# Optimization experiments

Measured on AMD Instinct MI355X. Metric: run time of the kernel, lower is better.

## Reference

```python
import jax, jax.numpy as jnp
import numpy as np

NUM_LAYERS = 12
D = 256          # d_model
H = 8            # n_head
DK = D // H      # qk_dim = v_dim = 32
FFD = 1024       # ffd_dim
B, L = 32, 448
EPS = 1e-6
MAXLEN = 500


def _sinusoidal_pos_emb(maxlen, hidden_dim):
    depth = hidden_dim / 2
    positions = np.arange(maxlen, dtype=np.float32)[:, None]
    depths = np.arange(depth, dtype=np.float32)[None, :] / depth
    angle_rads = positions * (1.0 / np.power(10000.0, depths))
    pe = np.concatenate([np.sin(angle_rads), np.cos(angle_rads)], axis=-1)
    return jnp.asarray(pe, jnp.float32)


def setup_inputs() -> dict:
    key = jax.random.key(0)
    ks = jax.random.split(key, 16)
    s = 0.02
    inp = {
        "x": jax.random.normal(ks[0], (B, L, D), jnp.float32),
        "mask": jnp.zeros((B, L), jnp.bool_),
        "pos_emb": _sinusoidal_pos_emb(MAXLEN - 1, D)[:L],  # [L, D]
        "Wq": jax.random.normal(ks[1], (NUM_LAYERS, D, D), jnp.float32) * s,
        "bq": jnp.zeros((NUM_LAYERS, D), jnp.float32),
        "Wk": jax.random.normal(ks[2], (NUM_LAYERS, D, D), jnp.float32) * s,
        "bk": jnp.zeros((NUM_LAYERS, D), jnp.float32),
        "Wv": jax.random.normal(ks[3], (NUM_LAYERS, D, D), jnp.float32) * s,
        "bv": jnp.zeros((NUM_LAYERS, D), jnp.float32),
        "Wo": jax.random.normal(ks[4], (NUM_LAYERS, D, D), jnp.float32) * s,
        "bo": jnp.zeros((NUM_LAYERS, D), jnp.float32),
        "W1": jax.random.normal(ks[5], (NUM_LAYERS, D, FFD), jnp.float32) * s,
        "bf1": jnp.zeros((NUM_LAYERS, FFD), jnp.float32),
        "W2": jax.random.normal(ks[6], (NUM_LAYERS, FFD, D), jnp.float32) * s,
        "bf2": jnp.zeros((NUM_LAYERS, D), jnp.float32),
        "ln1_g": jnp.ones((NUM_LAYERS, D), jnp.float32),
        "ln1_b": jnp.zeros((NUM_LAYERS, D), jnp.float32),
        "ln2_g": jnp.ones((NUM_LAYERS, D), jnp.float32),
        "ln2_b": jnp.zeros((NUM_LAYERS, D), jnp.float32),
    }
    return inp


def _layer_norm(x, g, b):
    mu = jnp.mean(x, axis=-1, keepdims=True)
    var = jnp.mean(jnp.square(x - mu), axis=-1, keepdims=True)
    return (x - mu) * jax.lax.rsqrt(var + EPS) * g + b


def _encoder_forward(x, mask, pos_emb, Wq, bq, Wk, bk, Wv, bv, Wo, bo,
                     W1, bf1, W2, bf2, ln1_g, ln1_b, ln2_g, ln2_b):
    Bx, Lx, _ = x.shape
    scale = 1.0 / np.sqrt(DK)
    x = x + pos_emb[None, :Lx, :]
    mask_b = mask[:, None, None, :]  # [B,1,1,L], True = masked
    for i in range(NUM_LAYERS):
        # --- pre-norm attention ---
        nx = _layer_norm(x, ln1_g[i], ln1_b[i])
        q = (nx @ Wq[i] + bq[i]).reshape(Bx, Lx, H, DK)
        k = (nx @ Wk[i] + bk[i]).reshape(Bx, Lx, H, DK)
        v = (nx @ Wv[i] + bv[i]).reshape(Bx, Lx, H, DK)
        dot = jnp.einsum("bihd,bjhd->bhij", q, k) * scale
        dot = jnp.where(mask_b, -10000.0, dot)
        attn = jax.nn.softmax(dot, axis=-1)
        o = jnp.einsum("bhij,bjhd->bihd", attn, v).reshape(Bx, Lx, D)
        x = x + (o @ Wo[i] + bo[i])
        # --- pre-norm FFN (exact GELU, as torch nn.GELU) ---
        nx2 = _layer_norm(x, ln2_g[i], ln2_b[i])
        h = jax.nn.gelu(nx2 @ W1[i] + bf1[i], approximate=False)
        x = x + (h @ W2[i] + bf2[i])
    return x


def reference(x, mask, pos_emb, Wq, bq, Wk, bk, Wv, bv, Wo, bo,
              W1, bf1, W2, bf2, ln1_g, ln1_b, ln2_g, ln2_b):
    return _encoder_forward(x, mask, pos_emb, Wq, bq, Wk, bk, Wv, bv, Wo, bo,
                            W1, bf1, W2, bf2, ln1_g, ln1_b, ln2_g, ln2_b)
```

## Files before the change

kernel.cpp:

```cpp
#include <hip/hip_runtime.h>

#define NL 12
#define DM 256
#define FFDIM 1024
#define BBATCH 32
#define LSEQ 448
#define MTOK (BBATCH*LSEQ)
#define EPSF 1e-6f

typedef __attribute__((ext_vector_type(8))) short bf16x8;
typedef __attribute__((ext_vector_type(4))) float f32x4;
typedef unsigned short u16;
typedef unsigned int u32;

__device__ __forceinline__ u16 f2bf(float f) {
    union { float f; u32 u; } v; v.f = f;
    u32 r = v.u + 0x7fffu + ((v.u >> 16) & 1u);
    return (u16)(r >> 16);
}
__device__ __forceinline__ float gelu_exact(float x) {
    return 0.5f * x * (1.0f + erff(x * 0.70710678118654752f));
}
__device__ __forceinline__ void gload16(const u16* g, u16* l) {
    __builtin_amdgcn_global_load_lds(
        (const __attribute__((address_space(1))) u32*)g,
        (__attribute__((address_space(3))) u32*)l, 16, 0, 0);
}

__global__ __launch_bounds__(256) void add_pos_k(
    const float* __restrict__ x, const float* __restrict__ pe, float* __restrict__ out)
{
    int i = blockIdx.x * 256 + threadIdx.x;
    float4 xv = ((const float4*)x)[i];
    float4 pv = ((const float4*)pe)[i % (LSEQ * DM / 4)];
    float4 r;
    r.x = xv.x + pv.x; r.y = xv.y + pv.y; r.z = xv.z + pv.z; r.w = xv.w + pv.w;
    ((float4*)out)[i] = r;
}

__global__ __launch_bounds__(256) void ln_k(
    const float* __restrict__ x, const float* __restrict__ g,
    const float* __restrict__ b, u16* __restrict__ out)
{
    const int w = threadIdx.x >> 6, lane = threadIdx.x & 63;
    const int row = blockIdx.x * 4 + w;
    float4 v = ((const float4*)(x + (size_t)row * DM))[lane];
    float s = v.x + v.y + v.z + v.w;
#pragma unroll
    for (int off = 32; off; off >>= 1) s += __shfl_xor(s, off);
    float mu = s * (1.0f / 256.0f);
    float d0 = v.x - mu, d1 = v.y - mu, d2 = v.z - mu, d3 = v.w - mu;
    float sq = d0*d0 + d1*d1 + d2*d2 + d3*d3;
#pragma unroll
    for (int off = 32; off; off >>= 1) sq += __shfl_xor(sq, off);
    float rs = rsqrtf(sq * (1.0f / 256.0f) + EPSF);
    float4 gv = ((const float4*)g)[lane];
    float4 bv = ((const float4*)b)[lane];
    ushort4 o;
    o.x = f2bf(d0 * rs * gv.x + bv.x);
    o.y = f2bf(d1 * rs * gv.y + bv.y);
    o.z = f2bf(d2 * rs * gv.z + bv.z);
    o.w = f2bf(d3 * rs * gv.w + bv.w);
    *(ushort4*)(out + (size_t)row * DM + lane * 4) = o;
}

__global__ __launch_bounds__(256) void twt_k(
    const float* __restrict__ in, u16* __restrict__ out,
    int K, int N, int in_lstride, int out_lstride)
{
    __shared__ float tl[32][33];
    const int l = blockIdx.z;
    const int n0 = blockIdx.x * 32, k0 = blockIdx.y * 32;
    const int tx = threadIdx.x & 31, ty = threadIdx.x >> 5;
    const float* src = in + (size_t)l * in_lstride;
#pragma unroll
    for (int i = 0; i < 4; ++i)
        tl[ty + 8*i][tx] = src[(size_t)(k0 + ty + 8*i) * N + n0 + tx];
    __syncthreads();
    u16* dst = out + (size_t)l * out_lstride;
#pragma unroll
    for (int i = 0; i < 4; ++i)
        dst[(size_t)(n0 + ty + 8*i) * K + k0 + tx] = f2bf(tl[tx][ty + 8*i]);
}

__global__ __launch_bounds__(256) void pack_bias_k(
    const float* __restrict__ bq, const float* __restrict__ bk,
    const float* __restrict__ bv, float* __restrict__ bqkv)
{
    int i = blockIdx.x * 256 + threadIdx.x;
    if (i >= NL * 768) return;
    int l = i / 768, c = i % 768;
    float v = (c < 256) ? bq[l*256 + c] : (c < 512) ? bk[l*256 + c - 256] : bv[l*256 + c - 512];
    bqkv[i] = v;
}

__global__ __launch_bounds__(256) void vt_k(
    const u16* __restrict__ qkv, u16* __restrict__ vtg)
{
    __shared__ u16 tl[32][33];
    const int kt = blockIdx.x, h = blockIdx.y, b = blockIdx.z;
    const int tx = threadIdx.x & 31, ty = threadIdx.x >> 5;
#pragma unroll
    for (int i = 0; i < 4; ++i)
        tl[ty + 8*i][tx] = qkv[(size_t)(b*LSEQ + kt*32 + ty + 8*i) * 768 + 512 + h*32 + tx];
    __syncthreads();
#pragma unroll
    for (int i = 0; i < 4; ++i)
        vtg[((size_t)(b*8 + h)*32 + ty + 8*i) * 448 + kt*32 + tx] = tl[tx][ty + 8*i];
}

template<int BN, int EPI>
__global__ __launch_bounds__(256, 2) void mm_k(
    const u16* __restrict__ A, int lda, const u16* __restrict__ Bt,
    const float* __restrict__ bias, void* __restrict__ C, int ldc, int K)
{
    __shared__ u16 As[2 * 128 * 32];
    __shared__ u16 Bs[2 * BN * 32];
    constexpr int MT = (BN == 128) ? 4 : 2;
    constexpr int BPANEL = BN * 32;
    const int tid = threadIdx.x;
    const int by = blockIdx.x, bx = blockIdx.y;
    const int w = tid >> 6, lane = tid & 63;
    const int lm = lane & 15, lk = lane >> 4;
    const int wm = (BN == 128) ? (w >> 1) : w;
    const int wn = (BN == 128) ? (w & 1) : 0;
    const int m0 = wm * MT * 16;
    const int n0 = wn * 64;
    const int lrow = lane >> 2, lcol = (lane & 3) * 8;

    const u16* Ab = A + (size_t)(by * 128) * lda;
    const u16* Bb = Bt + (size_t)(bx * BN) * K;

    f32x4 zz = {0.f, 0.f, 0.f, 0.f};
    f32x4 acc[MT][4];
#pragma unroll
    for (int i = 0; i < MT; ++i)
#pragma unroll
        for (int j = 0; j < 4; ++j) acc[i][j] = zz;

    for (int k0 = 0; k0 < K; k0 += 64) {
        __syncthreads();
#pragma unroll
        for (int p = 0; p < 2; ++p) {
#pragma unroll
            for (int i = 0; i < 2; ++i) {
                int seg = w * 2 + i;
                gload16(Ab + (size_t)(seg * 16 + lrow) * lda + k0 + p * 32 + lcol,
                        &As[p * 4096 + seg * 512]);
            }
            if constexpr (BN == 128) {
#pragma unroll
                for (int i = 0; i < 2; ++i) {
                    int seg = w * 2 + i;
                    gload16(Bb + (size_t)(seg * 16 + lrow) * K + k0 + p * 32 + lcol,
                            &Bs[p * BPANEL + seg * 512]);
                }
            } else {
                gload16(Bb + (size_t)(w * 16 + lrow) * K + k0 + p * 32 + lcol,
                        &Bs[p * BPANEL + w * 512]);
            }
        }
        __syncthreads();

#pragma unroll
        for (int p = 0; p < 2; ++p) {
            bf16x8 af[MT], bfr[4];
#pragma unroll
            for (int mt = 0; mt < MT; ++mt)
                af[mt] = *(const bf16x8*)&As[p * 4096 + (m0 + mt*16 + lm)*32 + lk*8];
#pragma unroll
            for (int nt = 0; nt < 4; ++nt)
                bfr[nt] = *(const bf16x8*)&Bs[p * BPANEL + (n0 + nt*16 + lm)*32 + lk*8];
#pragma unroll
            for (int mt = 0; mt < MT; ++mt)
#pragma unroll
                for (int nt = 0; nt < 4; ++nt)
                    acc[mt][nt] = __builtin_amdgcn_mfma_f32_16x16x32_bf16(af[mt], bfr[nt], acc[mt][nt], 0, 0, 0);
        }
    }

    float bv[4];
#pragma unroll
    for (int nt = 0; nt < 4; ++nt) bv[nt] = bias[bx*BN + n0 + nt*16 + lm];
#pragma unroll
    for (int mt = 0; mt < MT; ++mt) {
#pragma unroll
        for (int r = 0; r < 4; ++r) {
            int grow = by*128 + m0 + mt*16 + lk*4 + r;
#pragma unroll
            for (int nt = 0; nt < 4; ++nt) {
                int gcol = bx*BN + n0 + nt*16 + lm;
                float vv = acc[mt][nt][r] + bv[nt];
                if constexpr (EPI == 0) {
                    ((u16*)C)[(size_t)grow * ldc + gcol] = f2bf(vv);
                } else if constexpr (EPI == 1) {
                    ((u16*)C)[(size_t)grow * ldc + gcol] = f2bf(gelu_exact(vv));
                } else {
                    float* p = (float*)C + (size_t)grow * ldc + gcol;
                    *p += vv;
                }
            }
        }
    }
}

__global__ __launch_bounds__(256, 2) void attn_k(
    const u16* __restrict__ qkv, const u16* __restrict__ vtg,
    const unsigned char* __restrict__ mask, u16* __restrict__ ob)
{
    __shared__ u16 Klds[448 * 32];
    __shared__ u16 Plds[4][16 * 68];
    const int tid = threadIdx.x, w = tid >> 6, lane = tid & 63;
    const int lm = lane & 15, lk = lane >> 4;
    const int bid = blockIdx.x;
    const int bh = bid & 255, sg = bid >> 8;
    const int b = bh >> 3, h = bh & 7;
    const size_t rowbase = (size_t)b * LSEQ;

#pragma unroll
    for (int i = 0; i < 7; ++i) {
        int seg = w * 7 + i;
        gload16(qkv + (rowbase + seg * 16 + (lane >> 2)) * 768 + 256 + h * 32 + (lane & 3) * 8,
                &Klds[seg * 512]);
    }
    unsigned mbits = 0;
#pragma unroll
    for (int t = 0; t < 28; ++t)
        mbits |= (mask[b * LSEQ + t * 16 + lm] ? 1u : 0u) << t;
    __syncthreads();

    const u16* Vb = vtg + (size_t)bh * 32 * 448;
    const float scale = 0.17677669529663687f;
    f32x4 zz = {0.f, 0.f, 0.f, 0.f};

    const int q0 = (sg * 4 + w) * 16;
    bf16x8 qf = *(const bf16x8*)(qkv + (rowbase + q0 + lm) * 768 + h * 32 + lk * 8);
    f32x4 sc[28];
#pragma unroll
    for (int t = 0; t < 28; ++t) {
        bf16x8 kf = *(const bf16x8*)&Klds[(t*16 + lm)*32 + lk*8];
        sc[t] = __builtin_amdgcn_mfma_f32_16x16x32_bf16(qf, kf, zz, 0, 0, 0);
    }
    float mx[4] = {-1e30f, -1e30f, -1e30f, -1e30f};
#pragma unroll
    for (int t = 0; t < 28; ++t) {
        bool m = (mbits >> t) & 1;
#pragma unroll
        for (int r = 0; r < 4; ++r) {
            float v = m ? -10000.0f : sc[t][r] * scale;
            sc[t][r] = v;
            mx[r] = fmaxf(mx[r], v);
        }
    }
#pragma unroll
    for (int off = 1; off < 16; off <<= 1)
#pragma unroll
        for (int r = 0; r < 4; ++r) mx[r] = fmaxf(mx[r], __shfl_xor(mx[r], off));
    float sum[4] = {0.f, 0.f, 0.f, 0.f};
#pragma unroll
    for (int t = 0; t < 28; ++t)
#pragma unroll
        for (int r = 0; r < 4; ++r) {
            float e = __expf(sc[t][r] - mx[r]);
            sc[t][r] = e;
            sum[r] += e;
        }
#pragma unroll
    for (int off = 1; off < 16; off <<= 1)
#pragma unroll
        for (int r = 0; r < 4; ++r) sum[r] += __shfl_xor(sum[r], off);
    float inv[4];
#pragma unroll
    for (int r = 0; r < 4; ++r) inv[r] = 1.0f / sum[r];

    f32x4 oacc[2] = {zz, zz};
    u16* P = &Plds[w][0];
#pragma unroll
    for (int cc = 0; cc < 7; ++cc) {
#pragma unroll
        for (int tt = 0; tt < 4; ++tt) {
            int t = cc*4 + tt;
#pragma unroll
            for (int r = 0; r < 4; ++r)
                P[(lk*4 + r)*68 + tt*16 + lm] = f2bf(sc[t][r]);
        }
        bf16x8 pa0 = *(const bf16x8*)&P[lm*68 + lk*8];
        bf16x8 pa1 = *(const bf16x8*)&P[lm*68 + 32 + lk*8];
#pragma unroll
        for (int dt = 0; dt < 2; ++dt) {
            bf16x8 vb0 = *(const bf16x8*)(Vb + (size_t)(dt*16 + lm)*448 + cc*64 + lk*8);
            bf16x8 vb1 = *(const bf16x8*)(Vb + (size_t)(dt*16 + lm)*448 + cc*64 + 32 + lk*8);
            oacc[dt] = __builtin_amdgcn_mfma_f32_16x16x32_bf16(pa0, vb0, oacc[dt], 0, 0, 0);
            oacc[dt] = __builtin_amdgcn_mfma_f32_16x16x32_bf16(pa1, vb1, oacc[dt], 0, 0, 0);
        }
    }
#pragma unroll
    for (int dt = 0; dt < 2; ++dt)
#pragma unroll
        for (int r = 0; r < 4; ++r)
            ob[(rowbase + q0 + lk*4 + r)*256 + h*32 + dt*16 + lm] = f2bf(oacc[dt][r] * inv[r]);
}

extern "C" void kernel_launch(void* const* d_in, const int* in_sizes, int n_in,
                              void* d_out, int out_size, void* d_ws, size_t ws_size,
                              hipStream_t stream)
{
    const float* x_in = (const float*)d_in[0];
    const unsigned char* mask = (const unsigned char*)d_in[1];
    const float* pe   = (const float*)d_in[2];
    const float* Wq = (const float*)d_in[3];
    const float* bq = (const float*)d_in[4];
    const float* Wk = (const float*)d_in[5];
    const float* bk = (const float*)d_in[6];
    const float* Wv = (const float*)d_in[7];
    const float* bv = (const float*)d_in[8];
    const float* Wo = (const float*)d_in[9];
    const float* bo = (const float*)d_in[10];
    const float* W1 = (const float*)d_in[11];
    const float* bf1 = (const float*)d_in[12];
    const float* W2 = (const float*)d_in[13];
    const float* bf2 = (const float*)d_in[14];
    const float* ln1_g = (const float*)d_in[15];
    const float* ln1_b = (const float*)d_in[16];
    const float* ln2_g = (const float*)d_in[17];
    const float* ln2_b = (const float*)d_in[18];

    float* x = (float*)d_out;
    u16* ws = (u16*)d_ws;
    u16* nx   = ws;
    u16* qkv  = nx + 3670016;
    u16* ob   = qkv + 11010048;
    u16* vtg  = ob + 3670016;
    u16* hb   = qkv;
    u16* wqkvt = vtg + 3670016;
    u16* wot  = wqkvt + 2359296;
    u16* w1t  = wot + 786432;
    u16* w2t  = w1t + 3145728;
    float* bqkv = (float*)(w2t + 3145728);

    add_pos_k<<<MTOK * DM / 1024, 256, 0, stream>>>(x_in, pe, x);

    twt_k<<<dim3(8, 8, NL), 256, 0, stream>>>(Wq, wqkvt,          256, 256, 65536, 196608);
    twt_k<<<dim3(8, 8, NL), 256, 0, stream>>>(Wk, wqkvt + 65536,  256, 256, 65536, 196608);
    twt_k<<<dim3(8, 8, NL), 256, 0, stream>>>(Wv, wqkvt + 131072, 256, 256, 65536, 196608);
    twt_k<<<dim3(8, 8, NL), 256, 0, stream>>>(Wo, wot, 256, 256, 65536, 65536);
    twt_k<<<dim3(32, 8, NL), 256, 0, stream>>>(W1, w1t, 256, 1024, 262144, 262144);
    twt_k<<<dim3(8, 32, NL), 256, 0, stream>>>(W2, w2t, 1024, 256, 262144, 262144);
    pack_bias_k<<<(NL * 768 + 255) / 256, 256, 0, stream>>>(bq, bk, bv, bqkv);

    for (int l = 0; l < NL; ++l) {
        ln_k<<<MTOK / 4, 256, 0, stream>>>(x, ln1_g + l*256, ln1_b + l*256, nx);
        mm_k<128, 0><<<dim3(112, 6), 256, 0, stream>>>(
            nx, 256, wqkvt + (size_t)l*196608, bqkv + l*768, qkv, 768, 256);
        vt_k<<<dim3(14, 8, 32), 256, 0, stream>>>(qkv, vtg);
        attn_k<<<1792, 256, 0, stream>>>(qkv, vtg, mask, ob);
        mm_k<64, 2><<<dim3(112, 4), 256, 0, stream>>>(
            ob, 256, wot + (size_t)l*65536, bo + l*256, x, 256, 256);
        ln_k<<<MTOK / 4, 256, 0, stream>>>(x, ln2_g + l*256, ln2_b + l*256, nx);
        mm_k<128, 1><<<dim3(112, 8), 256, 0, stream>>>(
            nx, 256, w1t + (size_t)l*262144, bf1 + l*1024, hb, 1024, 256);
        mm_k<64, 2><<<dim3(112, 4), 256, 0, stream>>>(
            hb, 1024, w2t + (size_t)l*262144, bf2 + l*256, x, 256, 1024);
    }
}
```

Measured before the change: 1.563 ms.

## Recompute attention scores to shrink registers, fold Q scale into QKV GEMM, retile residual GEMMs

The attention kernel stops holding all 28 score tiles in registers. It computes QK^T once to get the row max, then recomputes the scores while exponentiating and feeding P·V. This removes a separate exp pass, and launch bounds are raised to 4 blocks per CU for higher occupancy, at the cost of doubling the QK MFMAs. The 1/sqrt(dk) scale is moved into a new QKV GEMM epilogue that scales the Q columns. The Wo and W2 residual GEMMs switch to 64x64 tiles with twice as many blocks and higher occupancy bounds.

Measured after the change: 1.456 ms. -6.8%, faster.

```diff
diff --git a/kernel.cpp b/kernel.cpp
--- a/kernel.cpp
+++ b/kernel.cpp
@@ -7,6 +7,7 @@
 #define LSEQ 448
 #define MTOK (BBATCH*LSEQ)
 #define EPSF 1e-6f
+#define QSCALE 0.17677669529663687f
 
 typedef __attribute__((ext_vector_type(8))) short bf16x8;
 typedef __attribute__((ext_vector_type(4))) float f32x4;
@@ -109,26 +110,25 @@
         vtg[((size_t)(b*8 + h)*32 + ty + 8*i) * 448 + kt*32 + tx] = tl[tx][ty + 8*i];
 }
 
-template<int BN, int EPI>
-__global__ __launch_bounds__(256, 2) void mm_k(
+template<int BM, int BN, int EPI>
+__global__ __launch_bounds__(256, (BM == 64) ? 4 : 3) void mm_k(
     const u16* __restrict__ A, int lda, const u16* __restrict__ Bt,
     const float* __restrict__ bias, void* __restrict__ C, int ldc, int K)
 {
-    __shared__ u16 As[2 * 128 * 32];
+    __shared__ u16 As[2 * BM * 32];
     __shared__ u16 Bs[2 * BN * 32];
-    constexpr int MT = (BN == 128) ? 4 : 2;
+    constexpr int MT = (BM == 128) ? 4 : 1;
+    constexpr int APANEL = BM * 32;
     constexpr int BPANEL = BN * 32;
     const int tid = threadIdx.x;
     const int by = blockIdx.x, bx = blockIdx.y;
     const int w = tid >> 6, lane = tid & 63;
     const int lm = lane & 15, lk = lane >> 4;
-    const int wm = (BN == 128) ? (w >> 1) : w;
-    const int wn = (BN == 128) ? (w & 1) : 0;
-    const int m0 = wm * MT * 16;
-    const int n0 = wn * 64;
+    const int m0 = (BM == 128) ? ((w >> 1) * 64) : (w * 16);
+    const int n0 = (BM == 128) ? ((w & 1) * 64) : 0;
     const int lrow = lane >> 2, lcol = (lane & 3) * 8;
 
-    const u16* Ab = A + (size_t)(by * 128) * lda;
+    const u16* Ab = A + (size_t)(by * BM) * lda;
     const u16* Bb = Bt + (size_t)(bx * BN) * K;
 
     f32x4 zz = {0.f, 0.f, 0.f, 0.f};
@@ -142,20 +142,18 @@
         __syncthreads();
 #pragma unroll
         for (int p = 0; p < 2; ++p) {
-#pragma unroll
-            for (int i = 0; i < 2; ++i) {
-                int seg = w * 2 + i;
-                gload16(Ab + (size_t)(seg * 16 + lrow) * lda + k0 + p * 32 + lcol,
-                        &As[p * 4096 + seg * 512]);
-            }
-            if constexpr (BN == 128) {
+            if constexpr (BM == 128) {
 #pragma unroll
                 for (int i = 0; i < 2; ++i) {
                     int seg = w * 2 + i;
+                    gload16(Ab + (size_t)(seg * 16 + lrow) * lda + k0 + p * 32 + lcol,
+                            &As[p * APANEL + seg * 512]);
                     gload16(Bb + (size_t)(seg * 16 + lrow) * K + k0 + p * 32 + lcol,
                             &Bs[p * BPANEL + seg * 512]);
                 }
             } else {
+                gload16(Ab + (size_t)(w * 16 + lrow) * lda + k0 + p * 32 + lcol,
+                        &As[p * APANEL + w * 512]);
                 gload16(Bb + (size_t)(w * 16 + lrow) * K + k0 + p * 32 + lcol,
                         &Bs[p * BPANEL + w * 512]);
             }
@@ -167,7 +165,7 @@
             bf16x8 af[MT], bfr[4];
 #pragma unroll
             for (int mt = 0; mt < MT; ++mt)
-                af[mt] = *(const bf16x8*)&As[p * 4096 + (m0 + mt*16 + lm)*32 + lk*8];
+                af[mt] = *(const bf16x8*)&As[p * APANEL + (m0 + mt*16 + lm)*32 + lk*8];
 #pragma unroll
             for (int nt = 0; nt < 4; ++nt)
                 bfr[nt] = *(const bf16x8*)&Bs[p * BPANEL + (n0 + nt*16 + lm)*32 + lk*8];
@@ -186,7 +184,7 @@
     for (int mt = 0; mt < MT; ++mt) {
 #pragma unroll
         for (int r = 0; r < 4; ++r) {
-            int grow = by*128 + m0 + mt*16 + lk*4 + r;
+            int grow = by*BM + m0 + mt*16 + lk*4 + r;
 #pragma unroll
             for (int nt = 0; nt < 4; ++nt) {
                 int gcol = bx*BN + n0 + nt*16 + lm;
@@ -195,6 +193,9 @@
                     ((u16*)C)[(size_t)grow * ldc + gcol] = f2bf(vv);
                 } else if constexpr (EPI == 1) {
                     ((u16*)C)[(size_t)grow * ldc + gcol] = f2bf(gelu_exact(vv));
+                } else if constexpr (EPI == 3) {
+                    float qs = (gcol < 256) ? QSCALE : 1.0f;
+                    ((u16*)C)[(size_t)grow * ldc + gcol] = f2bf(vv * qs);
                 } else {
                     float* p = (float*)C + (size_t)grow * ldc + gcol;
                     *p += vv;
@@ -204,7 +205,7 @@
     }
 }
 
-__global__ __launch_bounds__(256, 2) void attn_k(
+__global__ __launch_bounds__(256, 4) void attn_k(
     const u16* __restrict__ qkv, const u16* __restrict__ vtg,
     const unsigned char* __restrict__ mask, u16* __restrict__ ob)
 {
@@ -230,25 +231,20 @@
     __syncthreads();
 
     const u16* Vb = vtg + (size_t)bh * 32 * 448;
-    const float scale = 0.17677669529663687f;
     f32x4 zz = {0.f, 0.f, 0.f, 0.f};
 
     const int q0 = (sg * 4 + w) * 16;
     bf16x8 qf = *(const bf16x8*)(qkv + (rowbase + q0 + lm) * 768 + h * 32 + lk * 8);
-    f32x4 sc[28];
+
+    float mx[4] = {-1e30f, -1e30f, -1e30f, -1e30f};
 #pragma unroll
     for (int t = 0; t < 28; ++t) {
         bf16x8 kf = *(const bf16x8*)&Klds[(t*16 + lm)*32 + lk*8];
-        sc[t] = __builtin_amdgcn_mfma_f32_16x16x32_bf16(qf, kf, zz, 0, 0, 0);
-    }
-    float mx[4] = {-1e30f, -1e30f, -1e30f, -1e30f};
-#pragma unroll
-    for (int t = 0; t < 28; ++t) {
+        f32x4 s = __builtin_amdgcn_mfma_f32_16x16x32_bf16(qf, kf, zz, 0, 0, 0);
         bool m = (mbits >> t) & 1;
 #pragma unroll
         for (int r = 0; r < 4; ++r) {
-            float v = m ? -10000.0f : sc[t][r] * scale;
-            sc[t][r] = v;
+            float v = m ? -10000.0f : s[r];
             mx[r] = fmaxf(mx[r], v);
         }
     }
@@ -256,33 +252,25 @@
     for (int off = 1; off < 16; off <<= 1)
 #pragma unroll
         for (int r = 0; r < 4; ++r) mx[r] = fmaxf(mx[r], __shfl_xor(mx[r], off));
+
+    f32x4 oacc[2] = {zz, zz};
     float sum[4] = {0.f, 0.f, 0.f, 0.f};
-#pragma unroll
-    for (int t = 0; t < 28; ++t)
-#pragma unroll
-        for (int r = 0; r < 4; ++r) {
-            float e = __expf(sc[t][r] - mx[r]);
-            sc[t][r] = e;
-            sum[r] += e;
-        }
-#pragma unroll
-    for (int off = 1; off < 16; off <<= 1)
-#pragma unroll
-        for (int r = 0; r < 4; ++r) sum[r] += __shfl_xor(sum[r], off);
-    float inv[4];
-#pragma unroll
-    for (int r = 0; r < 4; ++r) inv[r] = 1.0f / sum[r];
-
-    f32x4 oacc[2] = {zz, zz};
     u16* P = &Plds[w][0];
 #pragma unroll
     for (int cc = 0; cc < 7; ++cc) {
 #pragma unroll
         for (int tt = 0; tt < 4; ++tt) {
             int t = cc*4 + tt;
-#pragma unroll
-            for (int r = 0; r < 4; ++r)
-                P[(lk*4 + r)*68 + tt*16 + lm] = f2bf(sc[t][r]);
+            bf16x8 kf = *(const bf16x8*)&Klds[(t*16 + lm)*32 + lk*8];
+            f32x4 s = __builtin_amdgcn_mfma_f32_16x16x32_bf16(qf, kf, zz, 0, 0, 0);
+            bool m = (mbits >> t) & 1;
+#pragma unroll
+            for (int r = 0; r < 4; ++r) {
+                float v = m ? -10000.0f : s[r];
+                float e = __expf(v - mx[r]);
+                sum[r] += e;
+                P[(lk*4 + r)*68 + tt*16 + lm] = f2bf(e);
+            }
         }
         bf16x8 pa0 = *(const bf16x8*)&P[lm*68 + lk*8];
         bf16x8 pa1 = *(const bf16x8*)&P[lm*68 + 32 + lk*8];
@@ -294,6 +282,14 @@
             oacc[dt] = __builtin_amdgcn_mfma_f32_16x16x32_bf16(pa1, vb1, oacc[dt], 0, 0, 0);
         }
     }
+#pragma unroll
+    for (int off = 1; off < 16; off <<= 1)
+#pragma unroll
+        for (int r = 0; r < 4; ++r) sum[r] += __shfl_xor(sum[r], off);
+    float inv[4];
+#pragma unroll
+    for (int r = 0; r < 4; ++r) inv[r] = 1.0f / sum[r];
+
 #pragma unroll
     for (int dt = 0; dt < 2; ++dt)
 #pragma unroll
@@ -350,16 +346,16 @@
 
     for (int l = 0; l < NL; ++l) {
         ln_k<<<MTOK / 4, 256, 0, stream>>>(x, ln1_g + l*256, ln1_b + l*256, nx);
-        mm_k<128, 0><<<dim3(112, 6), 256, 0, stream>>>(
+        mm_k<128, 128, 3><<<dim3(112, 6), 256, 0, stream>>>(
             nx, 256, wqkvt + (size_t)l*196608, bqkv + l*768, qkv, 768, 256);
         vt_k<<<dim3(14, 8, 32), 256, 0, stream>>>(qkv, vtg);
         attn_k<<<1792, 256, 0, stream>>>(qkv, vtg, mask, ob);
-        mm_k<64, 2><<<dim3(112, 4), 256, 0, stream>>>(
+        mm_k<64, 64, 2><<<dim3(224, 4), 256, 0, stream>>>(
             ob, 256, wot + (size_t)l*65536, bo + l*256, x, 256, 256);
         ln_k<<<MTOK / 4, 256, 0, stream>>>(x, ln2_g + l*256, ln2_b + l*256, nx);
-        mm_k<128, 1><<<dim3(112, 8), 256, 0, stream>>>(
+        mm_k<128, 128, 1><<<dim3(112, 8), 256, 0, stream>>>(
             nx, 256, w1t + (size_t)l*262144, bf1 + l*1024, hb, 1024, 256);
-        mm_k<64, 2><<<dim3(112, 4), 256, 0, stream>>>(
+        mm_k<64, 64, 2><<<dim3(224, 4), 256, 0, stream>>>(
             hb, 1024, w2t + (size_t)l*262144, bf2 + l*256, x, 256, 1024);
     }
 }
```
